# Kernel tuning notes

Hardware: AMD Instinct MI355X
Metric: run time of the kernel (lower is better)

## Reference

```python
import jax, jax.numpy as jnp
import numpy as np
import math

H_IMG, W_IMG = 800, 1216
STRIDES = [4, 8, 16, 32, 64]
SIZES = [32, 64, 128, 256, 512]
RATIOS = [0.5, 1.0, 2.0]
NUM_PER_LEVEL = [(-(-H_IMG // s)) * (-(-W_IMG // s)) * len(RATIOS) for s in STRIDES]
A_TOTAL = sum(NUM_PER_LEVEL)  # 728973
B = 4
PRE_NMS = 1000   # pre_nms_top_n['testing']
POST_NMS = 1000  # post_nms_top_n['testing']
NMS_TH = 0.7
MIN_SIZE = 1e-3
BBOX_XFORM_CLIP = math.log(1000.0 / 16)
NEG = -1e10
LEVELS_NP = np.repeat(np.arange(len(NUM_PER_LEVEL)), NUM_PER_LEVEL).astype(np.int32)


def _make_anchors():
    out = []
    for stride, size in zip(STRIDES, SIZES):
        fh, fw = -(-H_IMG // stride), -(-W_IMG // stride)
        r = np.sqrt(np.asarray(RATIOS, dtype=np.float64))
        ws, hs = size / r, size * r
        base = np.stack([-ws / 2, -hs / 2, ws / 2, hs / 2], axis=1)  # [3,4]
        sx = np.arange(fw, dtype=np.float64) * stride
        sy = np.arange(fh, dtype=np.float64) * stride
        gy, gx = np.meshgrid(sy, sx, indexing='ij')
        shifts = np.stack([gx.ravel(), gy.ravel(), gx.ravel(), gy.ravel()], axis=1)
        out.append((shifts[:, None, :] + base[None]).reshape(-1, 4))
    return np.concatenate(out, 0).astype(np.float32)


def setup_inputs() -> dict:
    key = jax.random.key(0)
    k1, k2 = jax.random.split(key)
    objectness = jax.random.normal(k1, (B, A_TOTAL), dtype=jnp.float32)
    deltas = jax.random.normal(k2, (B, A_TOTAL, 4), dtype=jnp.float32) * 0.2
    anchors = jnp.asarray(_make_anchors())
    return {'objectness': objectness, 'deltas': deltas, 'anchors': anchors}


def _decode(deltas, anchors):
    # BoxCoder.decode with weights (1,1,1,1)
    wa = anchors[:, 2] - anchors[:, 0]
    ha = anchors[:, 3] - anchors[:, 1]
    cxa = anchors[:, 0] + 0.5 * wa
    cya = anchors[:, 1] + 0.5 * ha
    dx, dy = deltas[..., 0], deltas[..., 1]
    dw = jnp.minimum(deltas[..., 2], BBOX_XFORM_CLIP)
    dh = jnp.minimum(deltas[..., 3], BBOX_XFORM_CLIP)
    cx = dx * wa + cxa
    cy = dy * ha + cya
    w = jnp.exp(dw) * wa
    h = jnp.exp(dh) * ha
    return jnp.stack([cx - 0.5 * w, cy - 0.5 * h, cx + 0.5 * w, cy + 0.5 * h], axis=-1)


def _topk_per_level(obj):
    # _get_top_n_idx: independent top-k within each anchor level, indices offset
    idxs, off = [], 0
    for n in NUM_PER_LEVEL:
        k = min(PRE_NMS, n)
        _, ti = jax.lax.top_k(obj[:, off:off + n], k)
        idxs.append(ti + off)
        off += n
    return jnp.concatenate(idxs, axis=1)


def _pairwise_iou(b):
    area = (b[:, 2] - b[:, 0]) * (b[:, 3] - b[:, 1])
    lt = jnp.maximum(b[:, None, :2], b[None, :, :2])
    rb = jnp.minimum(b[:, None, 2:], b[None, :, 2:])
    wh = jnp.clip(rb - lt, 0.0)
    inter = wh[..., 0] * wh[..., 1]
    return inter / (area[:, None] + area[None, :] - inter)


def _filter_image(boxes, scores, lvl):
    # clip_boxes_to_image
    x1 = jnp.clip(boxes[:, 0], 0.0, W_IMG)
    y1 = jnp.clip(boxes[:, 1], 0.0, H_IMG)
    x2 = jnp.clip(boxes[:, 2], 0.0, W_IMG)
    y2 = jnp.clip(boxes[:, 3], 0.0, H_IMG)
    boxes = jnp.stack([x1, y1, x2, y2], axis=1)
    # remove_small_boxes (as a validity mask; fixed shapes under jit)
    valid = ((x2 - x1) >= MIN_SIZE) & ((y2 - y1) >= MIN_SIZE)
    scores = jnp.where(valid, scores, NEG)
    N = boxes.shape[0]
    # batched_nms: offset boxes per level so levels never overlap
    sg_boxes = jax.lax.stop_gradient(boxes)
    offset = lvl.astype(boxes.dtype) * (sg_boxes.max() + 1.0)
    order = jnp.argsort(-jax.lax.stop_gradient(scores))
    iou = _pairwise_iou(sg_boxes[order] + offset[order][:, None])  # [N,N]
    idx = jnp.arange(N)
    def body(i, keep):
        sup = (iou[i] > NMS_TH) & keep[i] & (idx > i)
        return keep & ~sup
    keep = jax.lax.fori_loop(0, N, body, valid[order])
    # kept entries in score order, then truncate to POST_NMS (fixed shape)
    prio = jnp.where(keep, idx, N)
    sel = jnp.argsort(prio)[:POST_NMS]
    kept = keep[sel]
    src = order[sel]
    out_b = jnp.where(kept[:, None], boxes[src], 0.0)
    out_s = jnp.where(kept, scores[src], NEG)
    return out_b, out_s


def reference(objectness, deltas, anchors):
    proposals = _decode(deltas, anchors)                      # [B,A,4]
    top_idx = _topk_per_level(objectness)                     # [B,5000]
    obj_sel = jnp.take_along_axis(objectness, top_idx, axis=1)
    prop_sel = jnp.take_along_axis(proposals, top_idx[..., None], axis=1)
    lvl_sel = jnp.asarray(LEVELS_NP)[top_idx]
    boxes, scores = jax.vmap(_filter_image)(prop_sel, obj_sel, lvl_sel)
    return boxes, scores  # [B,POST_NMS,4], [B,POST_NMS]
```

## Files before the change

### kernel.cpp

```cpp
#include <hip/hip_runtime.h>
#include <stdint.h>

#pragma clang fp contract(off)

#define B_IMGS   4
#define NLVL     5
#define A_TOTAL  242991
#define NSEL     4741
#define NBUCK    8192
#define BSHIFT   19
#define CAND_CAP 2048
#define POST_NMS 1000
#define NBL      (B_IMGS * NLVL)
#define NMS_TH   0.7f
#define NEGV     (-1e10f)
#define W_IMGF   1216.0f
#define H_IMGF   800.0f
#define MIN_SZ   1e-3f
#define BBOX_CLIP 4.135166556742356f

__device__ __forceinline__ int level_of(int a) {
    if (a < 182400) return 0;
    if (a < 228000) return 1;
    if (a < 239400) return 2;
    if (a < 242250) return 3;
    return 4;
}
__device__ __forceinline__ int lvl_k(int l) { return (l == 4) ? 741 : 1000; }

__device__ __forceinline__ unsigned flipf(float f) {
    unsigned u = __float_as_uint(f);
    return u ^ (unsigned)(((int)u >> 31) | 0x80000000);
}
__device__ __forceinline__ float unflipf(unsigned os) {
    unsigned u = (os & 0x80000000u) ? (os ^ 0x80000000u) : ~os;
    return __uint_as_float(u);
}

__device__ __forceinline__ void async_cp16(const void* g, void* l) {
    __builtin_amdgcn_global_load_lds(
        (const __attribute__((address_space(1))) unsigned*)g,
        (__attribute__((address_space(3))) unsigned*)l,
        16, 0, 0);
}

static constexpr size_t SZ_HIST    = (size_t)NBL * NBUCK * sizeof(unsigned);
static constexpr size_t OFF_CNT    = SZ_HIST;
static constexpr size_t OFF_BOXMAX = OFF_CNT + NBL * sizeof(unsigned);
static constexpr size_t ZERO_BYTES = OFF_BOXMAX + B_IMGS * sizeof(unsigned);
static constexpr size_t OFF_THR    = ZERO_BYTES;
static constexpr size_t OFF_CAND   = OFF_THR + NBL * sizeof(unsigned);
static constexpr size_t OFF_SEL    = OFF_CAND + (size_t)NBL * CAND_CAP * 8;
static constexpr size_t OFF_BOXR   = OFF_SEL + (size_t)B_IMGS * NSEL * 8;
static constexpr size_t OFF_SCR    = OFF_BOXR + (size_t)B_IMGS * NSEL * 16;
static constexpr size_t OFF_BOXL   = OFF_SCR + (size_t)B_IMGS * NSEL * 4;
static constexpr size_t OFF_VAL    = OFF_BOXL + (size_t)B_IMGS * NSEL * 16;
static constexpr size_t OFF_RMAP   = OFF_VAL + (size_t)B_IMGS * NSEL * 4;
static constexpr size_t OFF_KEEP   = OFF_RMAP + (size_t)B_IMGS * NSEL * 4;
static constexpr size_t OFF_MASK   = OFF_KEEP + (size_t)B_IMGS * NSEL * 4;
static constexpr size_t WS_NEED    = OFF_MASK + (size_t)NBL * 1024 * 16 * 8;

#define HBLK_PER_IMG 34
__global__ void k_hist(const float* __restrict__ obj, unsigned* __restrict__ hist) {
    __shared__ unsigned lh[NBUCK];
    const int tid = threadIdx.x;
    const int b = blockIdx.x / HBLK_PER_IMG;
    const int r = blockIdx.x - b * HBLK_PER_IMG;
    int l, sub, chunk, lstart, n;
    if (r < 24)      { l = 0; sub = r;      chunk = 7600; lstart = 0;      n = 182400; }
    else if (r < 30) { l = 1; sub = r - 24; chunk = 7600; lstart = 182400; n = 45600; }
    else if (r < 32) { l = 2; sub = r - 30; chunk = 5700; lstart = 228000; n = 11400; }
    else if (r == 32){ l = 3; sub = 0;      chunk = 2850; lstart = 239400; n = 2850; }
    else             { l = 4; sub = 0;      chunk = 741;  lstart = 242250; n = 741; }
    #pragma unroll
    for (int i = tid; i < NBUCK; i += 256) lh[i] = 0;
    __syncthreads();
    const int s0 = sub * chunk;
    const int cnt = min(chunk, n - s0);
    const float* src = obj + (size_t)b * A_TOTAL + lstart + s0;
    for (int i = tid; i < cnt; i += 256) {
        unsigned os = flipf(src[i]);
        atomicAdd(&lh[os >> BSHIFT], 1u);
    }
    __syncthreads();
    unsigned* gh = hist + (size_t)(b * NLVL + l) * NBUCK;
    for (int i = tid; i < NBUCK; i += 256) {
        unsigned v = lh[i];
        if (v) atomicAdd(&gh[i], v);
    }
}

__global__ void k_thresh(const unsigned* __restrict__ hist, unsigned* __restrict__ thr) {
    int bl = blockIdx.x;
    int l = bl % NLVL;
    int kl = lvl_k(l);
    int tid = threadIdx.x;
    __shared__ unsigned part[256];
    __shared__ unsigned chunkbuf[32];
    __shared__ int s_chunk;
    __shared__ unsigned s_cum;
    const unsigned* h = hist + (size_t)bl * NBUCK;
    unsigned s = 0;
    for (int i = 0; i < 32; ++i) s += h[tid * 32 + i];
    part[tid] = s;
    __syncthreads();
    if (tid == 0) {
        unsigned cum = 0;
        int t = 255;
        for (; t > 0; --t) {
            if (cum + part[t] >= (unsigned)kl) break;
            cum += part[t];
        }
        s_chunk = t;
        s_cum = cum;
    }
    __syncthreads();
    if (tid < 32) chunkbuf[tid] = h[s_chunk * 32 + tid];
    __syncthreads();
    if (tid == 0) {
        unsigned c2 = s_cum;
        int T = s_chunk * 32;
        for (int i = 31; i >= 0; --i) {
            c2 += chunkbuf[i];
            if (c2 >= (unsigned)kl) { T = s_chunk * 32 + i; break; }
        }
        thr[bl] = (unsigned)T;
    }
}

#define CBLK_PER_IMG 65
__global__ void k_compact(const float* __restrict__ obj, const unsigned* __restrict__ thr,
                          unsigned* __restrict__ cnt, unsigned long long* __restrict__ cand) {
    __shared__ unsigned long long sbuf[CAND_CAP];
    __shared__ unsigned lcnt;
    __shared__ unsigned gbase;
    const int tid = threadIdx.x;
    const int b = blockIdx.x / CBLK_PER_IMG;
    const int r = blockIdx.x - b * CBLK_PER_IMG;
    int l, sub, chunk, lstart, n;
    if (r < 48)      { l = 0; sub = r;      chunk = 3800; lstart = 0;      n = 182400; }
    else if (r < 60) { l = 1; sub = r - 48; chunk = 3800; lstart = 182400; n = 45600; }
    else if (r < 63) { l = 2; sub = r - 60; chunk = 3800; lstart = 228000; n = 11400; }
    else if (r == 63){ l = 3; sub = 0;      chunk = 2850; lstart = 239400; n = 2850; }
    else             { l = 4; sub = 0;      chunk = 741;  lstart = 242250; n = 741; }
    if (tid == 0) lcnt = 0;
    __syncthreads();
    const int bl = b * NLVL + l;
    const unsigned T = thr[bl];
    const int s0 = sub * chunk;
    const int m = min(chunk, n - s0);
    const int abase = lstart + s0;
    const float* src = obj + (size_t)b * A_TOTAL + abase;
    for (int i = tid; i < m; i += 256) {
        unsigned os = flipf(src[i]);
        if ((os >> BSHIFT) >= T) {
            unsigned slot = atomicAdd(&lcnt, 1u);
            if (slot < CAND_CAP)
                sbuf[slot] = (((unsigned long long)(~os)) << 32) | (unsigned)(abase + i);
        }
    }
    __syncthreads();
    unsigned total = lcnt; if (total > CAND_CAP) total = CAND_CAP;
    if (tid == 0) gbase = atomicAdd(&cnt[bl], total);
    __syncthreads();
    const unsigned gb = gbase;
    for (unsigned i = tid; i < total; i += 256) {
        unsigned g = gb + i;
        if (g < CAND_CAP)
            cand[(size_t)bl * CAND_CAP + g] = sbuf[i];
    }
}

__global__ void k_sortlevel(const unsigned long long* __restrict__ cand,
                            const unsigned* __restrict__ cnt,
                            unsigned long long* __restrict__ sel) {
    __shared__ unsigned long long keys[CAND_CAP];
    const int bl = blockIdx.x;
    const int b = bl / NLVL, l = bl - (bl / NLVL) * NLVL;
    const int tid = threadIdx.x;
    int m = (int)cnt[bl];
    if (m > CAND_CAP) m = CAND_CAP;
    for (int i = tid; i < CAND_CAP; i += 512)
        keys[i] = (i < m) ? cand[(size_t)bl * CAND_CAP + i] : ~0ULL;
    __syncthreads();
    for (int k = 2; k <= CAND_CAP; k <<= 1) {
        for (int j = k >> 1; j > 0; j >>= 1) {
            for (int t = tid; t < CAND_CAP / 2; t += 512) {
                int i = ((t / j) * (j << 1)) + (t % j);
                int p = i + j;
                bool up = ((i & k) == 0);
                unsigned long long a = keys[i], c = keys[p];
                if ((a > c) == up) { keys[i] = c; keys[p] = a; }
            }
            __syncthreads();
        }
    }
    int kl = lvl_k(l);
    for (int q = tid; q < kl; q += 512)
        sel[(size_t)b * NSEL + l * 1000 + q] = keys[q];
}

__device__ __forceinline__ int lbound_lds(const unsigned long long* s, int len,
                                          unsigned long long key) {
    int lo = 0, hi = len;
    while (lo < hi) {
        int mid = (lo + hi) >> 1;
        if (s[mid] < key) lo = mid + 1; else hi = mid;
    }
    return lo;
}

__global__ void k_decode(const float* __restrict__ deltas, const float* __restrict__ anchors,
                         const unsigned long long* __restrict__ sel,
                         float* __restrict__ boxes_r, float* __restrict__ score_r,
                         float* __restrict__ boxes_l, int* __restrict__ valid_l,
                         int* __restrict__ rankmap, unsigned* __restrict__ boxmax) {
    __shared__ unsigned long long skey[NSEL];
    __shared__ float wmax[4];
    const int b = blockIdx.y;
    const int tid = threadIdx.x;
    for (int i = tid; i < NSEL; i += 256)
        skey[i] = sel[(size_t)b * NSEL + i];
    __syncthreads();

    int p = blockIdx.x * 256 + tid;
    bool on = p < NSEL;
    float mx = 0.0f;
    if (on) {
        int l = p / 1000;
        int q = p - l * 1000;
        unsigned long long key = skey[p];
        unsigned a = (unsigned)(key & 0xFFFFFFFFu);
        unsigned os = ~((unsigned)(key >> 32));
        if (a >= A_TOTAL) a = 0;
        float score = unflipf(os);
        int r = q;
        for (int l2 = 0; l2 < NLVL; ++l2) {
            if (l2 == l) continue;
            r += lbound_lds(skey + l2 * 1000, lvl_k(l2), key);
        }
        const float* dv = deltas + ((size_t)b * A_TOTAL + a) * 4;
        const float* av = anchors + (size_t)a * 4;
        float ax1 = av[0], ay1 = av[1], ax2 = av[2], ay2 = av[3];
        float wa = ax2 - ax1, ha = ay2 - ay1;
        float cxa = ax1 + 0.5f * wa, cya = ay1 + 0.5f * ha;
        float dx = dv[0], dy = dv[1];
        float dw = fminf(dv[2], BBOX_CLIP), dh = fminf(dv[3], BBOX_CLIP);
        float cx = dx * wa + cxa, cy = dy * ha + cya;
        float w = expf(dw) * wa, h = expf(dh) * ha;
        float x1 = cx - 0.5f * w, y1 = cy - 0.5f * h;
        float x2 = cx + 0.5f * w, y2 = cy + 0.5f * h;
        float x1c = fminf(fmaxf(x1, 0.0f), W_IMGF);
        float y1c = fminf(fmaxf(y1, 0.0f), H_IMGF);
        float x2c = fminf(fmaxf(x2, 0.0f), W_IMGF);
        float y2c = fminf(fmaxf(y2, 0.0f), H_IMGF);
        int valid = ((x2c - x1c) >= MIN_SZ) && ((y2c - y1c) >= MIN_SZ);
        mx = fmaxf(fmaxf(x1c, y1c), fmaxf(x2c, y2c));
        size_t rp = (size_t)b * NSEL + r;
        boxes_r[rp * 4 + 0] = x1c; boxes_r[rp * 4 + 1] = y1c;
        boxes_r[rp * 4 + 2] = x2c; boxes_r[rp * 4 + 3] = y2c;
        score_r[rp] = score;
        size_t pp = (size_t)b * NSEL + p;
        boxes_l[pp * 4 + 0] = x1c; boxes_l[pp * 4 + 1] = y1c;
        boxes_l[pp * 4 + 2] = x2c; boxes_l[pp * 4 + 3] = y2c;
        valid_l[pp] = valid;
        rankmap[pp] = r;
    }
    #pragma unroll
    for (int o = 32; o > 0; o >>= 1)
        mx = fmaxf(mx, __shfl_xor(mx, o));
    if ((tid & 63) == 0) wmax[tid >> 6] = mx;
    __syncthreads();
    if (tid == 0) {
        float m2 = fmaxf(fmaxf(wmax[0], wmax[1]), fmaxf(wmax[2], wmax[3]));
        atomicMax(boxmax + b, __float_as_uint(m2));
    }
}

__global__ void k_mask(const float* __restrict__ boxes_l, const unsigned* __restrict__ boxmax,
                       unsigned long long* __restrict__ mask) {
    int bl = blockIdx.z;
    int b = bl / NLVL, l = bl - b * NLVL;
    int kl = lvl_k(l);
    int w = blockIdx.x, rt = blockIdx.y, tid = threadIdx.x;
    float M = __uint_as_float(boxmax[b]) + 1.0f;
    float off = (float)l * M;
    __shared__ float cb[64][5];
    int j0 = w * 64;
    int j = j0 + tid;
    if (j < kl) {
        const float* bp = boxes_l + ((size_t)b * NSEL + l * 1000 + j) * 4;
        float x1 = bp[0] + off, y1 = bp[1] + off, x2 = bp[2] + off, y2 = bp[3] + off;
        cb[tid][0] = x1; cb[tid][1] = y1; cb[tid][2] = x2; cb[tid][3] = y2;
        cb[tid][4] = (x2 - x1) * (y2 - y1);
    }
    __syncthreads();
    int i = rt * 64 + tid;
    if (i >= kl) return;
    unsigned long long word = 0;
    if (j0 + 63 > i) {
        const float* bp = boxes_l + ((size_t)b * NSEL + l * 1000 + i) * 4;
        float ix1 = bp[0] + off, iy1 = bp[1] + off, ix2 = bp[2] + off, iy2 = bp[3] + off;
        float ai = (ix2 - ix1) * (iy2 - iy1);
        int jmax = min(64, kl - j0);
        for (int bb = 0; bb < jmax; ++bb) {
            int jj = j0 + bb;
            if (jj <= i) continue;
            float ltx = fmaxf(ix1, cb[bb][0]), lty = fmaxf(iy1, cb[bb][1]);
            float rbx = fminf(ix2, cb[bb][2]), rby = fminf(iy2, cb[bb][3]);
            float ww = fmaxf(rbx - ltx, 0.0f), hh = fmaxf(rby - lty, 0.0f);
            float inter = ww * hh;
            float iou = inter / ((ai + cb[bb][4]) - inter);
            if (iou > NMS_TH) word |= (1ULL << bb);
        }
    }
    mask[((size_t)bl * 1024 + i) * 16 + w] = word;
}

__global__ void k_resolve(const int* __restrict__ valid_l, const int* __restrict__ rankmap,
                          const unsigned long long* __restrict__ mask, int* __restrict__ keep_r) {
    const int bl = blockIdx.x;
    const int b = bl / NLVL, l = bl - b * NLVL;
    const int kl = lvl_k(l);
    const int lane = threadIdx.x;
    __shared__ __align__(16) unsigned long long sbufA[64 * 16];
    __shared__ __align__(16) unsigned long long sbufB[64 * 16];
    const int base = b * NSEL + l * 1000;

    unsigned long long keep_w = 0;
    for (int c = 0; c < 16; ++c) {
        int q = c * 64 + lane;
        int vv = (q < kl) ? valid_l[base + q] : 0;
        unsigned long long bm = __ballot(vv);
        if (lane == c) keep_w = bm;
    }

    const int nch = (kl + 63) >> 6;
    const char* mbyte = (const char*)(mask + (size_t)bl * 1024 * 16);

    {
        const char* g0 = mbyte + (size_t)lane * 16;
        #pragma unroll
        for (int j = 0; j < 8; ++j)
            async_cp16(g0 + j * 1024, (char*)sbufA + j * 1024);
    }

    for (int c = 0; c < nch; ++c) {
        unsigned long long* cur = (c & 1) ? sbufB : sbufA;
        unsigned long long* nxt = (c & 1) ? sbufA : sbufB;
        __syncthreads();
        if (c + 1 < nch) {
            const char* g1 = mbyte + (size_t)(c + 1) * 8192 + (size_t)lane * 16;
            #pragma unroll
            for (int j = 0; j < 8; ++j)
                async_cp16(g1 + j * 1024, (char*)nxt + j * 1024);
        }
        unsigned long long kw = __shfl(keep_w, c);
        if (kw) {
            unsigned long long diag = cur[lane * 16 + c];
            unsigned dlo = (unsigned)diag, dhi = (unsigned)(diag >> 32);
            unsigned long long nz = __ballot(diag != 0ULL);
            unsigned long long rem = kw & nz;
            while (rem) {
                int r = __ffsll((long long)rem) - 1;
                unsigned lo = __builtin_amdgcn_readlane(dlo, r);
                unsigned hi = __builtin_amdgcn_readlane(dhi, r);
                unsigned long long d = ((unsigned long long)hi << 32) | lo;
                kw &= ~d;
                rem &= ~(d | (1ULL << r));
            }
            unsigned long long supp = 0;
            if (lane < 16) {
                #pragma unroll
                for (int r = 0; r < 64; ++r) {
                    unsigned long long m = cur[r * 16 + lane];
                    supp |= (((kw >> r) & 1ULL) ? m : 0ULL);
                }
            }
            if (lane == c) keep_w = kw;
            else if (lane < 16 && lane > c) keep_w &= ~supp;
        }
    }
    __syncthreads();
    for (int c = 0; c < 16; ++c) {
        unsigned long long kwc = __shfl(keep_w, c);
        int q = c * 64 + lane;
        if (q < kl)
            keep_r[b * NSEL + rankmap[base + q]] = (int)((kwc >> lane) & 1ULL);
    }
}

__global__ void k_output(const int* __restrict__ keep_r, const float* __restrict__ boxes_r,
                         const float* __restrict__ score_r, float* __restrict__ out) {
    int b = blockIdx.x, tid = threadIdx.x;
    float* ob = out + (size_t)b * POST_NMS * 4;
    float* osc = out + (size_t)B_IMGS * POST_NMS * 4 + (size_t)b * POST_NMS;
    for (int p = tid; p < POST_NMS; p += 256) {
        ob[p * 4 + 0] = 0.0f; ob[p * 4 + 1] = 0.0f;
        ob[p * 4 + 2] = 0.0f; ob[p * 4 + 3] = 0.0f;
        osc[p] = NEGV;
    }
    __syncthreads();
    const int CH = 19;
    int base = tid * CH;
    int cnt = 0;
    for (int k = 0; k < CH; ++k) {
        int r = base + k;
        if (r < NSEL) cnt += keep_r[b * NSEL + r];
    }
    __shared__ int ps[256];
    ps[tid] = cnt;
    __syncthreads();
    for (int ofs = 1; ofs < 256; ofs <<= 1) {
        int v = (tid >= ofs) ? ps[tid - ofs] : 0;
        __syncthreads();
        ps[tid] += v;
        __syncthreads();
    }
    int p = ps[tid] - cnt;
    for (int k = 0; k < CH; ++k) {
        int r = base + k;
        if (r < NSEL && keep_r[b * NSEL + r]) {
            if (p < POST_NMS) {
                const float* bp = boxes_r + ((size_t)b * NSEL + r) * 4;
                ob[p * 4 + 0] = bp[0]; ob[p * 4 + 1] = bp[1];
                ob[p * 4 + 2] = bp[2]; ob[p * 4 + 3] = bp[3];
                osc[p] = score_r[(size_t)b * NSEL + r];
            }
            ++p;
        }
    }
}

extern "C" void kernel_launch(void* const* d_in, const int* in_sizes, int n_in,
                              void* d_out, int out_size, void* d_ws, size_t ws_size,
                              hipStream_t stream) {
    const float* obj     = (const float*)d_in[0];
    const float* deltas  = (const float*)d_in[1];
    const float* anchors = (const float*)d_in[2];
    float* out = (float*)d_out;

    char* ws = (char*)d_ws;
    unsigned*            hist    = (unsigned*)(ws);
    unsigned*            cnt     = (unsigned*)(ws + OFF_CNT);
    unsigned*            boxmax  = (unsigned*)(ws + OFF_BOXMAX);
    unsigned*            thr     = (unsigned*)(ws + OFF_THR);
    unsigned long long*  cand    = (unsigned long long*)(ws + OFF_CAND);
    unsigned long long*  sel     = (unsigned long long*)(ws + OFF_SEL);
    float*               boxes_r = (float*)(ws + OFF_BOXR);
    float*               score_r = (float*)(ws + OFF_SCR);
    float*               boxes_l = (float*)(ws + OFF_BOXL);
    int*                 valid_l = (int*)(ws + OFF_VAL);
    int*                 rankmap = (int*)(ws + OFF_RMAP);
    int*                 keep_r  = (int*)(ws + OFF_KEEP);
    unsigned long long*  maskp   = (unsigned long long*)(ws + OFF_MASK);

    (void)in_sizes; (void)n_in; (void)out_size; (void)ws_size; (void)WS_NEED;

    hipMemsetAsync(d_ws, 0, ZERO_BYTES, stream);

    k_hist<<<B_IMGS * HBLK_PER_IMG, 256, 0, stream>>>(obj, hist);
    k_thresh<<<NBL, 256, 0, stream>>>(hist, thr);
    k_compact<<<B_IMGS * CBLK_PER_IMG, 256, 0, stream>>>(obj, thr, cnt, cand);
    k_sortlevel<<<NBL, 512, 0, stream>>>(cand, cnt, sel);
    k_decode<<<dim3((NSEL + 255) / 256, B_IMGS), 256, 0, stream>>>(
        deltas, anchors, sel, boxes_r, score_r, boxes_l, valid_l, rankmap, boxmax);
    k_mask<<<dim3(16, 16, NBL), 64, 0, stream>>>(boxes_l, boxmax, maskp);
    k_resolve<<<NBL, 64, 0, stream>>>(valid_l, rankmap, maskp, keep_r);
    k_output<<<B_IMGS, 256, 0, stream>>>(keep_r, boxes_r, score_r, out);
}
```

Measured before the change: 212.5 us.

## Fuse threshold search into compaction kernel and enlarge blocks for hist, decode, mask

Removes the separate threshold kernel. Each compaction block now recomputes its level's histogram threshold from the global histogram before filtering, which saves one launch and the threshold round-trip through global memory. It also raises block sizes: 512 threads for the histogram, 1024 for decode with 16 wave maxima, and 256-row groups for the mask kernel with early exit. The cost is redundant threshold computation in every compaction block and a bigger per-block load of the histogram.

```diff
diff --git a/kernel.cpp b/kernel.cpp
--- a/kernel.cpp
+++ b/kernel.cpp
@@ -19,13 +19,6 @@
 #define MIN_SZ   1e-3f
 #define BBOX_CLIP 4.135166556742356f
 
-__device__ __forceinline__ int level_of(int a) {
-    if (a < 182400) return 0;
-    if (a < 228000) return 1;
-    if (a < 239400) return 2;
-    if (a < 242250) return 3;
-    return 4;
-}
 __device__ __forceinline__ int lvl_k(int l) { return (l == 4) ? 741 : 1000; }
 
 __device__ __forceinline__ unsigned flipf(float f) {
@@ -48,8 +41,7 @@
 static constexpr size_t OFF_CNT    = SZ_HIST;
 static constexpr size_t OFF_BOXMAX = OFF_CNT + NBL * sizeof(unsigned);
 static constexpr size_t ZERO_BYTES = OFF_BOXMAX + B_IMGS * sizeof(unsigned);
-static constexpr size_t OFF_THR    = ZERO_BYTES;
-static constexpr size_t OFF_CAND   = OFF_THR + NBL * sizeof(unsigned);
+static constexpr size_t OFF_CAND   = (ZERO_BYTES + 15) & ~(size_t)15;
 static constexpr size_t OFF_SEL    = OFF_CAND + (size_t)NBL * CAND_CAP * 8;
 static constexpr size_t OFF_BOXR   = OFF_SEL + (size_t)B_IMGS * NSEL * 8;
 static constexpr size_t OFF_SCR    = OFF_BOXR + (size_t)B_IMGS * NSEL * 16;
@@ -73,67 +65,31 @@
     else if (r == 32){ l = 3; sub = 0;      chunk = 2850; lstart = 239400; n = 2850; }
     else             { l = 4; sub = 0;      chunk = 741;  lstart = 242250; n = 741; }
     #pragma unroll
-    for (int i = tid; i < NBUCK; i += 256) lh[i] = 0;
+    for (int i = tid; i < NBUCK; i += 512) lh[i] = 0;
     __syncthreads();
     const int s0 = sub * chunk;
     const int cnt = min(chunk, n - s0);
     const float* src = obj + (size_t)b * A_TOTAL + lstart + s0;
-    for (int i = tid; i < cnt; i += 256) {
+    for (int i = tid; i < cnt; i += 512) {
         unsigned os = flipf(src[i]);
         atomicAdd(&lh[os >> BSHIFT], 1u);
     }
     __syncthreads();
     unsigned* gh = hist + (size_t)(b * NLVL + l) * NBUCK;
-    for (int i = tid; i < NBUCK; i += 256) {
+    for (int i = tid; i < NBUCK; i += 512) {
         unsigned v = lh[i];
         if (v) atomicAdd(&gh[i], v);
     }
 }
 
-__global__ void k_thresh(const unsigned* __restrict__ hist, unsigned* __restrict__ thr) {
-    int bl = blockIdx.x;
-    int l = bl % NLVL;
-    int kl = lvl_k(l);
-    int tid = threadIdx.x;
+#define CBLK_PER_IMG 65
+__global__ void k_compact(const float* __restrict__ obj, const unsigned* __restrict__ hist,
+                          unsigned* __restrict__ cnt, unsigned long long* __restrict__ cand) {
+    __shared__ unsigned long long sbuf[CAND_CAP];
     __shared__ unsigned part[256];
     __shared__ unsigned chunkbuf[32];
     __shared__ int s_chunk;
-    __shared__ unsigned s_cum;
-    const unsigned* h = hist + (size_t)bl * NBUCK;
-    unsigned s = 0;
-    for (int i = 0; i < 32; ++i) s += h[tid * 32 + i];
-    part[tid] = s;
-    __syncthreads();
-    if (tid == 0) {
-        unsigned cum = 0;
-        int t = 255;
-        for (; t > 0; --t) {
-            if (cum + part[t] >= (unsigned)kl) break;
-            cum += part[t];
-        }
-        s_chunk = t;
-        s_cum = cum;
-    }
-    __syncthreads();
-    if (tid < 32) chunkbuf[tid] = h[s_chunk * 32 + tid];
-    __syncthreads();
-    if (tid == 0) {
-        unsigned c2 = s_cum;
-        int T = s_chunk * 32;
-        for (int i = 31; i >= 0; --i) {
-            c2 += chunkbuf[i];
-            if (c2 >= (unsigned)kl) { T = s_chunk * 32 + i; break; }
-        }
-        thr[bl] = (unsigned)T;
-    }
-}
-
-#define CBLK_PER_IMG 65
-__global__ void k_compact(const float* __restrict__ obj, const unsigned* __restrict__ thr,
-                          unsigned* __restrict__ cnt, unsigned long long* __restrict__ cand) {
-    __shared__ unsigned long long sbuf[CAND_CAP];
-    __shared__ unsigned lcnt;
-    __shared__ unsigned gbase;
+    __shared__ unsigned s_cum, s_thr, lcnt, gbase;
     const int tid = threadIdx.x;
     const int b = blockIdx.x / CBLK_PER_IMG;
     const int r = blockIdx.x - b * CBLK_PER_IMG;
@@ -143,10 +99,40 @@
     else if (r < 63) { l = 2; sub = r - 60; chunk = 3800; lstart = 228000; n = 11400; }
     else if (r == 63){ l = 3; sub = 0;      chunk = 2850; lstart = 239400; n = 2850; }
     else             { l = 4; sub = 0;      chunk = 741;  lstart = 242250; n = 741; }
+    const int bl = b * NLVL + l;
+    const int kl = lvl_k(l);
+    const unsigned* h = hist + (size_t)bl * NBUCK;
+    {
+        unsigned s = 0;
+        for (int i = 0; i < 32; ++i) s += h[tid * 32 + i];
+        part[tid] = s;
+    }
     if (tid == 0) lcnt = 0;
     __syncthreads();
-    const int bl = b * NLVL + l;
-    const unsigned T = thr[bl];
+    if (tid == 0) {
+        unsigned cum = 0;
+        int t = 255;
+        for (; t > 0; --t) {
+            if (cum + part[t] >= (unsigned)kl) break;
+            cum += part[t];
+        }
+        s_chunk = t;
+        s_cum = cum;
+    }
+    __syncthreads();
+    if (tid < 32) chunkbuf[tid] = h[s_chunk * 32 + tid];
+    __syncthreads();
+    if (tid == 0) {
+        unsigned c2 = s_cum;
+        int T = s_chunk * 32;
+        for (int i = 31; i >= 0; --i) {
+            c2 += chunkbuf[i];
+            if (c2 >= (unsigned)kl) { T = s_chunk * 32 + i; break; }
+        }
+        s_thr = (unsigned)T;
+    }
+    __syncthreads();
+    const unsigned T = s_thr;
     const int s0 = sub * chunk;
     const int m = min(chunk, n - s0);
     const int abase = lstart + s0;
@@ -216,14 +202,14 @@
                          float* __restrict__ boxes_l, int* __restrict__ valid_l,
                          int* __restrict__ rankmap, unsigned* __restrict__ boxmax) {
     __shared__ unsigned long long skey[NSEL];
-    __shared__ float wmax[4];
+    __shared__ float wmax[16];
     const int b = blockIdx.y;
     const int tid = threadIdx.x;
-    for (int i = tid; i < NSEL; i += 256)
+    for (int i = tid; i < NSEL; i += 1024)
         skey[i] = sel[(size_t)b * NSEL + i];
     __syncthreads();
 
-    int p = blockIdx.x * 256 + tid;
+    int p = blockIdx.x * 1024 + tid;
     bool on = p < NSEL;
     float mx = 0.0f;
     if (on) {
@@ -272,7 +258,9 @@
     if ((tid & 63) == 0) wmax[tid >> 6] = mx;
     __syncthreads();
     if (tid == 0) {
-        float m2 = fmaxf(fmaxf(wmax[0], wmax[1]), fmaxf(wmax[2], wmax[3]));
+        float m2 = wmax[0];
+        #pragma unroll
+        for (int i = 1; i < 16; ++i) m2 = fmaxf(m2, wmax[i]);
         atomicMax(boxmax + b, __float_as_uint(m2));
     }
 }
@@ -282,20 +270,23 @@
     int bl = blockIdx.z;
     int b = bl / NLVL, l = bl - b * NLVL;
     int kl = lvl_k(l);
-    int w = blockIdx.x, rt = blockIdx.y, tid = threadIdx.x;
+    int w = blockIdx.x, rg = blockIdx.y, tid = threadIdx.x;
+    if (rg * 256 >= kl) return;
     float M = __uint_as_float(boxmax[b]) + 1.0f;
     float off = (float)l * M;
     __shared__ float cb[64][5];
     int j0 = w * 64;
-    int j = j0 + tid;
-    if (j < kl) {
-        const float* bp = boxes_l + ((size_t)b * NSEL + l * 1000 + j) * 4;
-        float x1 = bp[0] + off, y1 = bp[1] + off, x2 = bp[2] + off, y2 = bp[3] + off;
-        cb[tid][0] = x1; cb[tid][1] = y1; cb[tid][2] = x2; cb[tid][3] = y2;
-        cb[tid][4] = (x2 - x1) * (y2 - y1);
-    }
-    __syncthreads();
-    int i = rt * 64 + tid;
+    if (tid < 64) {
+        int j = j0 + tid;
+        if (j < kl) {
+            const float* bp = boxes_l + ((size_t)b * NSEL + l * 1000 + j) * 4;
+            float x1 = bp[0] + off, y1 = bp[1] + off, x2 = bp[2] + off, y2 = bp[3] + off;
+            cb[tid][0] = x1; cb[tid][1] = y1; cb[tid][2] = x2; cb[tid][3] = y2;
+            cb[tid][4] = (x2 - x1) * (y2 - y1);
+        }
+    }
+    __syncthreads();
+    int i = rg * 256 + tid;
     if (i >= kl) return;
     unsigned long long word = 0;
     if (j0 + 63 > i) {
@@ -444,7 +435,6 @@
     unsigned*            hist    = (unsigned*)(ws);
     unsigned*            cnt     = (unsigned*)(ws + OFF_CNT);
     unsigned*            boxmax  = (unsigned*)(ws + OFF_BOXMAX);
-    unsigned*            thr     = (unsigned*)(ws + OFF_THR);
     unsigned long long*  cand    = (unsigned long long*)(ws + OFF_CAND);
     unsigned long long*  sel     = (unsigned long long*)(ws + OFF_SEL);
     float*               boxes_r = (float*)(ws + OFF_BOXR);
@@ -459,13 +449,12 @@
 
     hipMemsetAsync(d_ws, 0, ZERO_BYTES, stream);
 
-    k_hist<<<B_IMGS * HBLK_PER_IMG, 256, 0, stream>>>(obj, hist);
-    k_thresh<<<NBL, 256, 0, stream>>>(hist, thr);
-    k_compact<<<B_IMGS * CBLK_PER_IMG, 256, 0, stream>>>(obj, thr, cnt, cand);
+    k_hist<<<B_IMGS * HBLK_PER_IMG, 512, 0, stream>>>(obj, hist);
+    k_compact<<<B_IMGS * CBLK_PER_IMG, 256, 0, stream>>>(obj, hist, cnt, cand);
     k_sortlevel<<<NBL, 512, 0, stream>>>(cand, cnt, sel);
-    k_decode<<<dim3((NSEL + 255) / 256, B_IMGS), 256, 0, stream>>>(
+    k_decode<<<dim3(5, B_IMGS), 1024, 0, stream>>>(
         deltas, anchors, sel, boxes_r, score_r, boxes_l, valid_l, rankmap, boxmax);
-    k_mask<<<dim3(16, 16, NBL), 64, 0, stream>>>(boxes_l, boxmax, maskp);
+    k_mask<<<dim3(16, 4, NBL), 256, 0, stream>>>(boxes_l, boxmax, maskp);
     k_resolve<<<NBL, 64, 0, stream>>>(valid_l, rankmap, maskp, keep_r);
     k_output<<<B_IMGS, 256, 0, stream>>>(keep_r, boxes_r, score_r, out);
 }
```

Result: faster. 201.7 us (-5.1%).
